# Performance work log

Measured on AMD Instinct MI355X. Metric: run time of the kernel, lower is better.

## Reference

```python
import jax, jax.numpy as jnp
from jax import lax
import numpy as np

B0 = 2          # batch
S = 32          # spatial grid side; L = S*S + 2
L = S * S + 2
DM = 256        # d_model
ED = 512        # d_inner = expand_factor * d_model
N = 16          # d_state
R = 16          # dt_rank = ceil(d_model/16)
K = 4           # d_conv


def _dwconv(x, w, b):
    # x: (B, L, ED) -> causal depthwise conv1d, kernel K, left-pad K-1 (== torch pad K-1 then [:, :, :L])
    xt = jnp.transpose(x, (0, 2, 1))  # (B, ED, L)
    o = lax.conv_general_dilated(xt, w, (1,), [(K - 1, 0)],
                                 feature_group_count=ED,
                                 dimension_numbers=('NCH', 'OIH', 'NCH'))
    return jnp.transpose(o + b[None, :, None], (0, 2, 1))


def _ssm(x, Alog, Dp, xp_w, dt_w, dt_b):
    # x: (B, L, ED); selective scan (mamba.py math, pscan=True path)
    A = -jnp.exp(Alog)                       # (ED, N)
    dBC = x @ xp_w.T                          # (B, L, R+2N)
    delta = jax.nn.softplus(dBC[..., :R] @ dt_w.T + dt_b)  # (B, L, ED)
    Bm = dBC[..., R:R + N]                    # (B, L, N)
    Cm = dBC[..., R + N:]                     # (B, L, N)
    dA = jnp.exp(delta[..., None] * A)        # (B, L, ED, N)
    dBx = (delta * x)[..., None] * Bm[:, :, None, :]  # (B, L, ED, N)

    def comb(e1, e2):
        a1, b1 = e1
        a2, b2 = e2
        return a1 * a2, a2 * b1 + b2

    _, hs = lax.associative_scan(comb, (dA, dBx), axis=1)  # h_t = dA_t*h_{t-1} + dBx_t
    return jnp.einsum('blen,bln->ble', hs, Cm) + Dp * x


def _cross(t):
    # keep first/last token, transpose the SxS interior grid (row-major <-> col-major)
    b, l, d = t.shape
    inner = t[:, 1:-1].reshape(b, S, S, d).transpose(0, 2, 1, 3).reshape(b, S * S, d)
    return jnp.concatenate([t[:, :1], inner, t[:, -1:]], axis=1)


def _branch(xz, cw, cb, xp, dw, db, Al, Dp):
    xa, za = jnp.split(xz, 2, axis=-1)
    xa = jax.nn.silu(_dwconv(xa, cw, cb))
    return _ssm(xa, Al, Dp, xp, dw, db) * jax.nn.silu(za)


def _forward(x, in_w, out_w, *p):
    xz = x @ in_w.T  # (B, L, 2*ED)
    (cwa, cba, xpa, dwa, dba, Ala, Da,
     cwb, cbb, xpb, dwb, dbb, Alb, Db,
     cwc, cbc, xpc, dwc, dbc, Alc, Dc,
     cwd, cbd, xpd, dwd, dbd, Ald, Dd) = p
    ga = _branch(xz, cwa, cba, xpa, dwa, dba, Ala, Da)                # forward scan
    gb = _branch(xz[:, ::-1], cwb, cbb, xpb, dwb, dbb, Alb, Db)       # reversed scan
    xzc = _cross(xz)
    gc = _branch(xzc, cwc, cbc, xpc, dwc, dbc, Alc, Dc)               # transposed scan
    gd = _branch(xzc[:, ::-1], cwd, cbd, xpd, dwd, dbd, Ald, Dd)      # reversed-transposed scan
    # gating commutes with token permutations, so reassemble gated outputs
    y = (ga + gb[:, ::-1] + _cross(gc) + _cross(gd)[:, ::-1]) * 0.25  # divide_output=True
    return y @ out_w.T


def setup_inputs() -> dict:
    keys = jax.random.split(jax.random.key(0), 64)
    it = iter(keys)

    def nrm(shape, scale=0.02):
        return scale * jax.random.normal(next(it), shape, dtype=jnp.float32)

    d = {}
    d['x'] = jax.random.normal(next(it), (B0, L, DM), dtype=jnp.float32)
    d['in_w'] = nrm((2 * ED, DM))
    d['out_w'] = nrm((DM, ED))
    std = R ** -0.5
    for s in ['a', 'b', 'c', 'd']:
        d[f'conv_w_{s}'] = nrm((ED, 1, K), 0.1)
        d[f'conv_b_{s}'] = jnp.zeros((ED,), jnp.float32)
        d[f'xp_w_{s}'] = nrm((R + 2 * N, ED))
        d[f'dt_w_{s}'] = jax.random.uniform(next(it), (ED, R), minval=-std, maxval=std, dtype=jnp.float32)
        dt = jnp.exp(jax.random.uniform(next(it), (ED,), dtype=jnp.float32)
                     * (np.float32(np.log(0.1)) - np.float32(np.log(0.001))) + np.float32(np.log(0.001)))
        d[f'dt_b_{s}'] = dt + jnp.log(-jnp.expm1(-dt))  # inverse-softplus init
        d[f'Alog_{s}'] = jnp.log(jnp.tile(jnp.arange(1, N + 1, dtype=jnp.float32), (ED, 1)))
        d[f'D_{s}'] = jnp.ones((ED,), jnp.float32)
    return d


def reference(x, in_w, out_w,
              conv_w_a, conv_b_a, xp_w_a, dt_w_a, dt_b_a, Alog_a, D_a,
              conv_w_b, conv_b_b, xp_w_b, dt_w_b, dt_b_b, Alog_b, D_b,
              conv_w_c, conv_b_c, xp_w_c, dt_w_c, dt_b_c, Alog_c, D_c,
              conv_w_d, conv_b_d, xp_w_d, dt_w_d, dt_b_d, Alog_d, D_d):
    return _forward(x, in_w, out_w,
                    conv_w_a, conv_b_a, xp_w_a, dt_w_a, dt_b_a, Alog_a, D_a,
                    conv_w_b, conv_b_b, xp_w_b, dt_w_b, dt_b_b, Alog_b, D_b,
                    conv_w_c, conv_b_c, xp_w_c, dt_w_c, dt_b_c, Alog_c, D_c,
                    conv_w_d, conv_b_d, xp_w_d, dt_w_d, dt_b_d, Alog_d, D_d)
```

## Files before the change

kernel.cpp:

```cpp
#include <hip/hip_runtime.h>
#include <math.h>

#define LL 1026
#define EDim 512
#define MM 2052
#define NC 8
#define LC 128

struct Params {
  const float* cw[4];
  const float* cb[4];
  const float* xpw[4];
  const float* dtw[4];
  const float* dtb[4];
  const float* Al[4];
  const float* Dp[4];
};

__device__ __forceinline__ int sigma_map(int branch, int l) {
  if (branch & 1) l = LL - 1 - l;
  if (branch & 2) {
    if (l > 0 && l < LL - 1) {
      int p = l - 1;
      l = 1 + ((p & 31) << 5) + (p >> 5);
    }
  }
  return l;
}

__device__ __forceinline__ float silu_f(float v) {
  return v * __builtin_amdgcn_rcpf(1.f + __expf(-v));
}
__device__ __forceinline__ float softplus_f(float s) {
  return fmaxf(s, 0.f) + __logf(1.f + __expf(-fabsf(s)));
}

template<int CTRL>
__device__ __forceinline__ float dpp_mov0(float x) {
  int r = __builtin_amdgcn_update_dpp(0, __float_as_int(x), CTRL, 0xF, 0xF, false);
  return __int_as_float(r);
}

__global__ __launch_bounds__(256) void k1_gemm_in(
    const float* __restrict__ x, const float* __restrict__ w,
    float* __restrict__ xa, float* __restrict__ sz) {
  __shared__ float As[32][68];
  __shared__ float Bs[32][68];
  const int t = threadIdx.x;
  const int tx = t & 15, ty = t >> 4;
  const int m0 = blockIdx.x * 64, n0 = blockIdx.y * 64;
  float acc[4][4] = {};
  for (int k0 = 0; k0 < 256; k0 += 32) {
    #pragma unroll
    for (int p = 0; p < 2; ++p) {
      int f = t + p * 256;
      int row = f >> 3, cf = f & 7;
      int gr = m0 + row; gr = gr < MM ? gr : MM - 1;
      float4 v = *(const float4*)(x + (size_t)gr * 256 + k0 + cf * 4);
      As[cf*4+0][row] = v.x; As[cf*4+1][row] = v.y;
      As[cf*4+2][row] = v.z; As[cf*4+3][row] = v.w;
      int gn = n0 + row;
      float4 u = *(const float4*)(w + (size_t)gn * 256 + k0 + cf * 4);
      Bs[cf*4+0][row] = u.x; Bs[cf*4+1][row] = u.y;
      Bs[cf*4+2][row] = u.z; Bs[cf*4+3][row] = u.w;
    }
    __syncthreads();
    #pragma unroll
    for (int k = 0; k < 32; ++k) {
      float4 av = *(const float4*)&As[k][ty*4];
      float4 bv = *(const float4*)&Bs[k][tx*4];
      float a0 = av.x, a1 = av.y, a2 = av.z, a3 = av.w;
      float b0 = bv.x, b1 = bv.y, b2 = bv.z, b3 = bv.w;
      acc[0][0]=fmaf(a0,b0,acc[0][0]); acc[0][1]=fmaf(a0,b1,acc[0][1]); acc[0][2]=fmaf(a0,b2,acc[0][2]); acc[0][3]=fmaf(a0,b3,acc[0][3]);
      acc[1][0]=fmaf(a1,b0,acc[1][0]); acc[1][1]=fmaf(a1,b1,acc[1][1]); acc[1][2]=fmaf(a1,b2,acc[1][2]); acc[1][3]=fmaf(a1,b3,acc[1][3]);
      acc[2][0]=fmaf(a2,b0,acc[2][0]); acc[2][1]=fmaf(a2,b1,acc[2][1]); acc[2][2]=fmaf(a2,b2,acc[2][2]); acc[2][3]=fmaf(a2,b3,acc[2][3]);
      acc[3][0]=fmaf(a3,b0,acc[3][0]); acc[3][1]=fmaf(a3,b1,acc[3][1]); acc[3][2]=fmaf(a3,b2,acc[3][2]); acc[3][3]=fmaf(a3,b3,acc[3][3]);
    }
    __syncthreads();
  }
  #pragma unroll
  for (int i = 0; i < 4; ++i) {
    int gm = m0 + ty*4 + i;
    if (gm < MM) {
      #pragma unroll
      for (int j = 0; j < 4; ++j) {
        int gn = n0 + tx*4 + j;
        float v = acc[i][j];
        if (gn < 512) xa[(size_t)gm*512 + gn] = v;
        else          sz[(size_t)gm*512 + gn - 512] = silu_f(v);
      }
    }
  }
}

__global__ __launch_bounds__(256) void k2_branch(
    Params P, const float* __restrict__ xa,
    float* __restrict__ xac, float* __restrict__ delta, float* __restrict__ bcg,
    float* __restrict__ acc_out) {
  __shared__ float xcS[16][516];
  __shared__ float dBCs[16][49];
  const int t = threadIdx.x;
  const int l0 = blockIdx.x * 16;
  const int b  = blockIdx.y;
  const int br = blockIdx.z;
  const int e0 = 2 * t;

  if (br == 0) {
    float* ab = acc_out + ((size_t)b * LL + l0) * 512;
    int nmax = (LL - l0 < 16 ? LL - l0 : 16) * 512;
    for (int idx = t; idx < nmax; idx += 256) ab[idx] = 0.f;
  }

  const float* cw = P.cw[br];
  const float w00 = cw[e0*4+0], w01 = cw[e0*4+1], w02 = cw[e0*4+2], w03 = cw[e0*4+3];
  const float w10 = cw[(e0+1)*4+0], w11 = cw[(e0+1)*4+1], w12 = cw[(e0+1)*4+2], w13 = cw[(e0+1)*4+3];
  const float cb0 = P.cb[br][e0], cb1 = P.cb[br][e0+1];
  const float* xab = xa + (size_t)b * LL * 512;
  const size_t obase = (size_t)(br*2 + b) * LL;

  float h0x=0,h0y=0,h1x=0,h1y=0,h2x=0,h2y=0,h3x=0,h3y=0;
  for (int i = -3; i < 16; ++i) {
    int l = l0 + i;
    float cx = 0.f, cy = 0.f;
    if (l >= 0 && l < LL) {
      int pos = sigma_map(br, l);
      float2 v = *(const float2*)(xab + (size_t)pos * 512 + e0);
      cx = v.x; cy = v.y;
    }
    h0x=h1x; h0y=h1y; h1x=h2x; h1y=h2y; h2x=h3x; h2y=h3y; h3x=cx; h3y=cy;
    if (i >= 0) {
      float o0 = fmaf(w00,h0x, fmaf(w01,h1x, fmaf(w02,h2x, fmaf(w03,h3x, cb0))));
      float o1 = fmaf(w10,h0y, fmaf(w11,h1y, fmaf(w12,h2y, fmaf(w13,h3y, cb1))));
      o0 = silu_f(o0); o1 = silu_f(o1);
      *(float2*)&xcS[i][e0] = make_float2(o0, o1);
      if (l < LL)
        *(float2*)(xac + (obase + l) * 512 + e0) = make_float2(o0, o1);
    }
  }
  __syncthreads();

  const int rowi = t & 15;
  const int r0 = t >> 4;
  const float* xpw = P.xpw[br];
  const float4* xr4 = (const float4*)&xcS[rowi][0];
  const float4* wa = (const float4*)(xpw + (size_t)r0 * 512);
  const float4* wb = (const float4*)(xpw + (size_t)(r0 + 16) * 512);
  const float4* wc = (const float4*)(xpw + (size_t)(r0 + 32) * 512);
  float acc0 = 0.f, acc1 = 0.f, acc2 = 0.f;
  #pragma unroll 8
  for (int e4 = 0; e4 < 128; ++e4) {
    float4 xv = xr4[e4];
    float4 a = wa[e4], bb = wb[e4], c = wc[e4];
    acc0 = fmaf(xv.x,a.x, fmaf(xv.y,a.y, fmaf(xv.z,a.z, fmaf(xv.w,a.w, acc0))));
    acc1 = fmaf(xv.x,bb.x,fmaf(xv.y,bb.y,fmaf(xv.z,bb.z,fmaf(xv.w,bb.w,acc1))));
    acc2 = fmaf(xv.x,c.x, fmaf(xv.y,c.y, fmaf(xv.z,c.z, fmaf(xv.w,c.w, acc2))));
  }
  dBCs[rowi][r0]      = acc0;
  dBCs[rowi][r0 + 16] = acc1;
  dBCs[rowi][r0 + 32] = acc2;
  __syncthreads();

  for (int idx = t; idx < 512; idx += 256) {
    int row = idx >> 5, c = idx & 31;
    int l = l0 + row;
    if (l < LL) bcg[(obase + l)*32 + c] = dBCs[row][16 + c];
  }

  const float* dtw = P.dtw[br];
  float dw0[16], dw1[16];
  #pragma unroll
  for (int r = 0; r < 16; ++r) { dw0[r] = dtw[e0*16 + r]; dw1[r] = dtw[(e0+1)*16 + r]; }
  const float db0 = P.dtb[br][e0], db1 = P.dtb[br][e0+1];
  for (int row = 0; row < 16; ++row) {
    int l = l0 + row;
    if (l >= LL) break;
    float s0 = db0, s1 = db1;
    #pragma unroll
    for (int r = 0; r < 16; ++r) {
      float d = dBCs[row][r];
      s0 = fmaf(d, dw0[r], s0);
      s1 = fmaf(d, dw1[r], s1);
    }
    *(float2*)(delta + (obase + l)*512 + e0) = make_float2(softplus_f(s0), softplus_f(s1));
  }
}

__global__ __launch_bounds__(256) void k3a_chunk(
    Params P, const float* __restrict__ xac, const float* __restrict__ delta,
    const float* __restrict__ bcg, float* __restrict__ Pc, float* __restrict__ Qc) {
  __shared__ float dT[16][33], xT[16][33], bT[16][33];
  const int t = threadIdx.x;
  const int eL = t >> 4, n = t & 15;
  const int e0 = blockIdx.x * 16;
  const int b = blockIdx.y;
  const int br = blockIdx.z / NC, c = blockIdx.z % NC;
  const size_t sbase = (size_t)(br*2 + b) * LL;
  const float* dl = delta + sbase * 512;
  const float* xc = xac + sbase * 512;
  const float* bc = bcg + sbase * 32;
  const float A_en = -__expf(P.Al[br][(e0 + eL)*16 + n]);
  const int l0 = c * LC;
  const int lend = (c == NC-1) ? LL : (l0 + LC);
  float h = 0.f, dsum = 0.f;

  for (int c0 = l0; c0 < lend; c0 += 32) {
    #pragma unroll
    for (int p = 0; p < 2; ++p) {
      int idx = t + p*256;
      int s = idx >> 4, ee = idx & 15;
      int l = c0 + s;
      float dv = 0.f, xv = 0.f, bv = 0.f;
      if (l < lend) {
        dv = dl[(size_t)l*512 + e0 + ee];
        xv = xc[(size_t)l*512 + e0 + ee];
        bv = bc[l*32 + ee];
      }
      dT[ee][s] = dv; xT[ee][s] = xv; bT[ee][s] = bv;
    }
    __syncthreads();
    float da[32], dbx[32];
    #pragma unroll
    for (int s = 0; s < 32; ++s) {
      float d = dT[eL][s];
      da[s]  = __expf(d * A_en);
      dbx[s] = d * xT[eL][s] * bT[n][s];
      dsum += d;
    }
    #pragma unroll
    for (int s = 0; s < 32; ++s) h = fmaf(da[s], h, dbx[s]);
    __syncthreads();
  }
  size_t oi = ((((size_t)(br*2 + b)*NC + c)*32 + blockIdx.x)*256 + t);
  Pc[oi] = __expf(dsum * A_en);
  Qc[oi] = h;
}

__global__ __launch_bounds__(256) void k3b_scan(
    Params P, const float* __restrict__ xac, const float* __restrict__ delta,
    const float* __restrict__ bcg, const float* __restrict__ sz,
    const float* __restrict__ Pc, const float* __restrict__ Qc,
    float* __restrict__ acc_out) {
  __shared__ float dT[16][33], xT[16][33], bT[16][33], cT[16][33];
  __shared__ float ybuf[32][17];
  const int t = threadIdx.x;
  const int eL = t >> 4, n = t & 15;
  const int e0 = blockIdx.x * 16;
  const int b = blockIdx.y;
  const int br = blockIdx.z / NC, c = blockIdx.z % NC;
  const size_t sbase = (size_t)(br*2 + b) * LL;
  const float* dl = delta + sbase * 512;
  const float* xc = xac + sbase * 512;
  const float* bc = bcg + sbase * 32;
  const float A_en = -__expf(P.Al[br][(e0 + eL)*16 + n]);
  const float Dval = P.Dp[br][e0 + (t & 15)];
  const float* szb = sz + (size_t)b * LL * 512;
  float* ab = acc_out + (size_t)b * LL * 512;

  float h = 0.f;
  for (int cc = 0; cc < c; ++cc) {
    size_t ii = ((((size_t)(br*2 + b)*NC + cc)*32 + blockIdx.x)*256 + t);
    h = fmaf(Pc[ii], h, Qc[ii]);
  }

  const int l0c = c * LC;
  const int lend = (c == NC-1) ? LL : (l0c + LC);
  for (int c0 = l0c; c0 < lend; c0 += 32) {
    #pragma unroll
    for (int p = 0; p < 2; ++p) {
      int idx = t + p*256;
      int s = idx >> 4, ee = idx & 15;
      int l = c0 + s;
      float dv = 0.f, xv = 0.f, bv = 0.f, cv = 0.f;
      if (l < lend) {
        dv = dl[(size_t)l*512 + e0 + ee];
        xv = xc[(size_t)l*512 + e0 + ee];
        bv = bc[l*32 + ee];
        cv = bc[l*32 + 16 + ee];
      }
      dT[ee][s] = dv; xT[ee][s] = xv; bT[ee][s] = bv; cT[ee][s] = cv;
    }
    __syncthreads();

    float da[32], dbx[32], ccv[32];
    #pragma unroll
    for (int s = 0; s < 32; ++s) {
      float d  = dT[eL][s];
      float xv = xT[eL][s];
      da[s]  = __expf(d * A_en);
      dbx[s] = d * xv * bT[n][s];
      ccv[s] = cT[n][s];
    }
    #pragma unroll
    for (int s = 0; s < 32; ++s) {
      h = fmaf(da[s], h, dbx[s]);
      float r = h * ccv[s];
      r += dpp_mov0<0xB1>(r);
      r += dpp_mov0<0x4E>(r);
      r += dpp_mov0<0x114>(r);
      r += dpp_mov0<0x118>(r);
      if (n == 15) ybuf[s][eL] = r;
    }
    __syncthreads();

    #pragma unroll
    for (int p = 0; p < 2; ++p) {
      int idx = t + p*256;
      int s = idx >> 4, ee = idx & 15;
      int l = c0 + s;
      if (l < lend) {
        float yv = fmaf(Dval, xT[ee][s], ybuf[s][ee]);
        int pos = sigma_map(br, l);
        float szv = szb[(size_t)pos * 512 + e0 + ee];
        atomicAdd(ab + (size_t)pos * 512 + e0 + ee, 0.25f * yv * szv);
      }
    }
    __syncthreads();
  }
}

__global__ __launch_bounds__(256) void k4_gemm_out(
    const float* __restrict__ acc_in, const float* __restrict__ w,
    float* __restrict__ out) {
  __shared__ float As[32][38];
  __shared__ float Bs[32][38];
  const int t = threadIdx.x;
  const int tx = t & 15, ty = t >> 4;
  const int m0 = blockIdx.x * 32, n0 = blockIdx.y * 32;
  float acc[2][2] = {};
  for (int k0 = 0; k0 < 512; k0 += 32) {
    #pragma unroll
    for (int p = 0; p < 4; ++p) {
      int idx = t + p*256;
      int row = idx >> 5, kk = idx & 31;
      int gm = m0 + row; gm = gm < MM ? gm : MM - 1;
      As[kk][row] = acc_in[(size_t)gm*512 + k0 + kk];
    }
    #pragma unroll
    for (int p = 0; p < 4; ++p) {
      int idx = t + p*256;
      int row = idx >> 5, kk = idx & 31;
      Bs[kk][row] = w[(size_t)(n0 + row)*512 + k0 + kk];
    }
    __syncthreads();
    #pragma unroll
    for (int k = 0; k < 32; ++k) {
      float2 av = *(const float2*)&As[k][ty*2];
      float2 bv = *(const float2*)&Bs[k][tx*2];
      acc[0][0]=fmaf(av.x,bv.x,acc[0][0]); acc[0][1]=fmaf(av.x,bv.y,acc[0][1]);
      acc[1][0]=fmaf(av.y,bv.x,acc[1][0]); acc[1][1]=fmaf(av.y,bv.y,acc[1][1]);
    }
    __syncthreads();
  }
  #pragma unroll
  for (int i = 0; i < 2; ++i) {
    int gm = m0 + ty*2 + i;
    if (gm < MM) {
      #pragma unroll
      for (int j = 0; j < 2; ++j)
        out[(size_t)gm*256 + n0 + tx*2 + j] = acc[i][j];
    }
  }
}

extern "C" void kernel_launch(void* const* d_in, const int* in_sizes, int n_in,
                              void* d_out, int out_size, void* d_ws, size_t ws_size,
                              hipStream_t stream) {
  const float* x    = (const float*)d_in[0];
  const float* in_w = (const float*)d_in[1];
  const float* out_w= (const float*)d_in[2];
  Params prm;
  for (int s = 0; s < 4; ++s) {
    prm.cw[s]  = (const float*)d_in[3 + s*7 + 0];
    prm.cb[s]  = (const float*)d_in[3 + s*7 + 1];
    prm.xpw[s] = (const float*)d_in[3 + s*7 + 2];
    prm.dtw[s] = (const float*)d_in[3 + s*7 + 3];
    prm.dtb[s] = (const float*)d_in[3 + s*7 + 4];
    prm.Al[s]  = (const float*)d_in[3 + s*7 + 5];
    prm.Dp[s]  = (const float*)d_in[3 + s*7 + 6];
  }
  float* ws = (float*)d_ws;
  const size_t SZ1 = (size_t)MM * 512;
  float* xa   = ws;
  float* szp  = ws + SZ1;
  float* xac  = ws + 2*SZ1;
  float* dlt  = ws + 6*SZ1;
  float* bc   = ws + 10*SZ1;
  float* acc  = ws + 10*SZ1 + (size_t)4*MM*32;
  float* Pc = xa;
  float* Qc = xa + (size_t)8*NC*32*256;

  k1_gemm_in<<<dim3(33, 16), 256, 0, stream>>>(x, in_w, xa, szp);
  k2_branch <<<dim3(65, 2, 4), 256, 0, stream>>>(prm, xa, xac, dlt, bc, acc);
  k3a_chunk <<<dim3(32, 2, 4*NC), 256, 0, stream>>>(prm, xac, dlt, bc, Pc, Qc);
  k3b_scan  <<<dim3(32, 2, 4*NC), 256, 0, stream>>>(prm, xac, dlt, bc, szp, Pc, Qc, acc);
  k4_gemm_out<<<dim3(65, 8), 256, 0, stream>>>(acc, out_w, (float*)d_out);
}
```

Before: 300.4 us.

## Double scan chunk count and vectorize LDS staging in chunked selective scan

Splits the sequence into 16 chunks of 64 instead of 8 of 128, doubling the number of blocks in both scan passes. This shortens each block's serial recurrence, at the cost of a longer carry-in prefix loop and more Pc/Qc traffic. Global-to-shared loads become float4 with the rows padded to 36 so they can be read back as float4, and the compute loop drops its staging register arrays. Pc/Qc move to a separate workspace region after acc, since the larger buffers no longer fit where xa was.

```diff
diff --git a/kernel.cpp b/kernel.cpp
--- a/kernel.cpp
+++ b/kernel.cpp
@@ -4,8 +4,8 @@
 #define LL 1026
 #define EDim 512
 #define MM 2052
-#define NC 8
-#define LC 128
+#define NC 16
+#define LC 64
 
 struct Params {
   const float* cw[4];
@@ -39,6 +39,14 @@
 __device__ __forceinline__ float dpp_mov0(float x) {
   int r = __builtin_amdgcn_update_dpp(0, __float_as_int(x), CTRL, 0xF, 0xF, false);
   return __int_as_float(r);
+}
+
+__device__ __forceinline__ float red16(float r) {
+  r += dpp_mov0<0xB1>(r);
+  r += dpp_mov0<0x4E>(r);
+  r += dpp_mov0<0x114>(r);
+  r += dpp_mov0<0x118>(r);
+  return r;
 }
 
 __global__ __launch_bounds__(256) void k1_gemm_in(
@@ -188,7 +196,7 @@
 __global__ __launch_bounds__(256) void k3a_chunk(
     Params P, const float* __restrict__ xac, const float* __restrict__ delta,
     const float* __restrict__ bcg, float* __restrict__ Pc, float* __restrict__ Qc) {
-  __shared__ float dT[16][33], xT[16][33], bT[16][33];
+  __shared__ float dT[16][36], xT[16][36], bT[16][36];
   const int t = threadIdx.x;
   const int eL = t >> 4, n = t & 15;
   const int e0 = blockIdx.x * 16;
@@ -204,30 +212,36 @@
   float h = 0.f, dsum = 0.f;
 
   for (int c0 = l0; c0 < lend; c0 += 32) {
-    #pragma unroll
-    for (int p = 0; p < 2; ++p) {
-      int idx = t + p*256;
-      int s = idx >> 4, ee = idx & 15;
-      int l = c0 + s;
-      float dv = 0.f, xv = 0.f, bv = 0.f;
-      if (l < lend) {
-        dv = dl[(size_t)l*512 + e0 + ee];
-        xv = xc[(size_t)l*512 + e0 + ee];
-        bv = bc[l*32 + ee];
+    {
+      const int idx = t & 127;
+      const int s = idx >> 2, q = idx & 3;
+      const int l = c0 + s;
+      float4 v = make_float4(0.f,0.f,0.f,0.f);
+      if (t < 128) {
+        if (l < lend) v = *(const float4*)(dl + (size_t)l*512 + e0 + q*4);
+        dT[q*4+0][s]=v.x; dT[q*4+1][s]=v.y; dT[q*4+2][s]=v.z; dT[q*4+3][s]=v.w;
+        float4 u = make_float4(0.f,0.f,0.f,0.f);
+        if (l < lend) u = *(const float4*)(bc + (size_t)l*32 + q*4);
+        bT[q*4+0][s]=u.x; bT[q*4+1][s]=u.y; bT[q*4+2][s]=u.z; bT[q*4+3][s]=u.w;
+      } else {
+        if (l < lend) v = *(const float4*)(xc + (size_t)l*512 + e0 + q*4);
+        xT[q*4+0][s]=v.x; xT[q*4+1][s]=v.y; xT[q*4+2][s]=v.z; xT[q*4+3][s]=v.w;
       }
-      dT[ee][s] = dv; xT[ee][s] = xv; bT[ee][s] = bv;
-    }
-    __syncthreads();
-    float da[32], dbx[32];
-    #pragma unroll
-    for (int s = 0; s < 32; ++s) {
-      float d = dT[eL][s];
-      da[s]  = __expf(d * A_en);
-      dbx[s] = d * xT[eL][s] * bT[n][s];
-      dsum += d;
-    }
-    #pragma unroll
-    for (int s = 0; s < 32; ++s) h = fmaf(da[s], h, dbx[s]);
+    }
+    __syncthreads();
+    #pragma unroll
+    for (int s4 = 0; s4 < 32; s4 += 4) {
+      float4 dv = *(const float4*)&dT[eL][s4];
+      float4 xv = *(const float4*)&xT[eL][s4];
+      float4 bv = *(const float4*)&bT[n][s4];
+      float g0 = __expf(dv.x*A_en), g1 = __expf(dv.y*A_en);
+      float g2 = __expf(dv.z*A_en), g3 = __expf(dv.w*A_en);
+      dsum += (dv.x+dv.y)+(dv.z+dv.w);
+      h = fmaf(g0, h, dv.x*xv.x*bv.x);
+      h = fmaf(g1, h, dv.y*xv.y*bv.y);
+      h = fmaf(g2, h, dv.z*xv.z*bv.z);
+      h = fmaf(g3, h, dv.w*xv.w*bv.w);
+    }
     __syncthreads();
   }
   size_t oi = ((((size_t)(br*2 + b)*NC + c)*32 + blockIdx.x)*256 + t);
@@ -240,8 +254,8 @@
     const float* __restrict__ bcg, const float* __restrict__ sz,
     const float* __restrict__ Pc, const float* __restrict__ Qc,
     float* __restrict__ acc_out) {
-  __shared__ float dT[16][33], xT[16][33], bT[16][33], cT[16][33];
-  __shared__ float ybuf[32][17];
+  __shared__ float dT[16][36], xT[16][36], bT[16][36], cT[16][36];
+  __shared__ float yb[16][36];
   const int t = threadIdx.x;
   const int eL = t >> 4, n = t & 15;
   const int e0 = blockIdx.x * 16;
@@ -265,40 +279,45 @@
   const int l0c = c * LC;
   const int lend = (c == NC-1) ? LL : (l0c + LC);
   for (int c0 = l0c; c0 < lend; c0 += 32) {
-    #pragma unroll
-    for (int p = 0; p < 2; ++p) {
-      int idx = t + p*256;
-      int s = idx >> 4, ee = idx & 15;
-      int l = c0 + s;
-      float dv = 0.f, xv = 0.f, bv = 0.f, cv = 0.f;
-      if (l < lend) {
-        dv = dl[(size_t)l*512 + e0 + ee];
-        xv = xc[(size_t)l*512 + e0 + ee];
-        bv = bc[l*32 + ee];
-        cv = bc[l*32 + 16 + ee];
+    {
+      const int idx = t & 127;
+      const int s = idx >> 2, q = idx & 3;
+      const int l = c0 + s;
+      float4 v = make_float4(0.f,0.f,0.f,0.f);
+      if (t < 128) {
+        if (l < lend) v = *(const float4*)(dl + (size_t)l*512 + e0 + q*4);
+        dT[q*4+0][s]=v.x; dT[q*4+1][s]=v.y; dT[q*4+2][s]=v.z; dT[q*4+3][s]=v.w;
+      } else {
+        if (l < lend) v = *(const float4*)(xc + (size_t)l*512 + e0 + q*4);
+        xT[q*4+0][s]=v.x; xT[q*4+1][s]=v.y; xT[q*4+2][s]=v.z; xT[q*4+3][s]=v.w;
       }
-      dT[ee][s] = dv; xT[ee][s] = xv; bT[ee][s] = bv; cT[ee][s] = cv;
-    }
-    __syncthreads();
-
-    float da[32], dbx[32], ccv[32];
-    #pragma unroll
-    for (int s = 0; s < 32; ++s) {
-      float d  = dT[eL][s];
-      float xv = xT[eL][s];
-      da[s]  = __expf(d * A_en);
-      dbx[s] = d * xv * bT[n][s];
-      ccv[s] = cT[n][s];
-    }
-    #pragma unroll
-    for (int s = 0; s < 32; ++s) {
-      h = fmaf(da[s], h, dbx[s]);
-      float r = h * ccv[s];
-      r += dpp_mov0<0xB1>(r);
-      r += dpp_mov0<0x4E>(r);
-      r += dpp_mov0<0x114>(r);
-      r += dpp_mov0<0x118>(r);
-      if (n == 15) ybuf[s][eL] = r;
+    }
+    {
+      const int s = t >> 3, q = t & 7;
+      const int l = c0 + s;
+      float4 u = make_float4(0.f,0.f,0.f,0.f);
+      if (l < lend) u = *(const float4*)(bc + (size_t)l*32 + q*4);
+      if (q < 4) {
+        bT[q*4+0][s]=u.x; bT[q*4+1][s]=u.y; bT[q*4+2][s]=u.z; bT[q*4+3][s]=u.w;
+      } else {
+        int q4 = (q-4)*4;
+        cT[q4+0][s]=u.x; cT[q4+1][s]=u.y; cT[q4+2][s]=u.z; cT[q4+3][s]=u.w;
+      }
+    }
+    __syncthreads();
+
+    #pragma unroll
+    for (int s4 = 0; s4 < 32; s4 += 4) {
+      float4 dv = *(const float4*)&dT[eL][s4];
+      float4 xv = *(const float4*)&xT[eL][s4];
+      float4 bv = *(const float4*)&bT[n][s4];
+      float4 cv = *(const float4*)&cT[n][s4];
+      float r0, r1, r2, r3;
+      h = fmaf(__expf(dv.x*A_en), h, dv.x*xv.x*bv.x); r0 = red16(h*cv.x);
+      h = fmaf(__expf(dv.y*A_en), h, dv.y*xv.y*bv.y); r1 = red16(h*cv.y);
+      h = fmaf(__expf(dv.z*A_en), h, dv.z*xv.z*bv.z); r2 = red16(h*cv.z);
+      h = fmaf(__expf(dv.w*A_en), h, dv.w*xv.w*bv.w); r3 = red16(h*cv.w);
+      if (n == 15) *(float4*)&yb[eL][s4] = make_float4(r0, r1, r2, r3);
     }
     __syncthreads();
 
@@ -308,7 +327,7 @@
       int s = idx >> 4, ee = idx & 15;
       int l = c0 + s;
       if (l < lend) {
-        float yv = fmaf(Dval, xT[ee][s], ybuf[s][ee]);
+        float yv = fmaf(Dval, xT[ee][s], yb[ee][s]);
         int pos = sigma_map(br, l);
         float szv = szb[(size_t)pos * 512 + e0 + ee];
         atomicAdd(ab + (size_t)pos * 512 + e0 + ee, 0.25f * yv * szv);
@@ -386,8 +405,8 @@
   float* dlt  = ws + 6*SZ1;
   float* bc   = ws + 10*SZ1;
   float* acc  = ws + 10*SZ1 + (size_t)4*MM*32;
-  float* Pc = xa;
-  float* Qc = xa + (size_t)8*NC*32*256;
+  float* Pc   = acc + SZ1;
+  float* Qc   = Pc + (size_t)8*NC*32*256;
 
   k1_gemm_in<<<dim3(33, 16), 256, 0, stream>>>(x, in_w, xa, szp);
   k2_branch <<<dim3(65, 2, 4), 256, 0, stream>>>(prm, xa, xac, dlt, bc, acc);
```

Result: faster. 279.3 us (-7.0%).
